# Kernel tuning notes

Measured on AMD Instinct MI355X. Metric: run time of the kernel, lower is better.

Reference implementation:

```python
import jax, jax.numpy as jnp
import numpy as np
import math

PS = 16            # patch size for SigmaPredictor
HID = 8            # hidden_dim
SCALE = HID ** -0.5
SIGMA_CAP = 6.0    # BoundedSoftplus threshold
EPS_S = 1e-6       # BoundedSoftplus eps


def setup_inputs() -> dict:
    key = jax.random.key(0)
    ks = jax.random.split(key, 10)
    B, C, H, W = 2, 1, 384, 384
    d_in = C * PS * PS  # 256
    r = lambda k_, sh: jax.random.normal(k_, sh, dtype=jnp.float32) * 0.1
    z = lambda sh: jnp.zeros(sh, dtype=jnp.float32)
    return {
        "x": jax.random.uniform(ks[0], (B, C, H, W), dtype=jnp.float32),
        "Wq": r(ks[1], (d_in, HID)), "bq": z((HID,)),
        "Wk": r(ks[2], (d_in, HID)), "bk": z((HID,)),
        "Wv": r(ks[3], (d_in, HID)), "bv": z((HID,)),
        "Wsq": r(ks[4], (HID, HID)), "bsq": z((HID,)),
        "Wsk": r(ks[5], (HID, HID)), "bsk": z((HID,)),
        "Wsv": r(ks[6], (HID, HID)), "bsv": z((HID,)),
        "ln_g": jnp.ones((HID,), jnp.float32), "ln_b": z((HID,)),
        "Wp": r(ks[7], (HID, 3)),
        # bias ~4 -> sigmas ~4 -> kernel size k=13 (production-scale support)
        "bp": jnp.full((3,), 4.0, dtype=jnp.float32),
    }


def _attn(q, k, v):
    a = jax.nn.softmax(jnp.einsum('bnd,bmd->bnm', q, k) * SCALE, axis=-1)
    return jnp.einsum('bnm,bmd->bnd', a, v)


def _predict_sigmas(x, Wq, bq, Wk, bk, Wv, bv, Wsq, bsq, Wsk, bsk, Wsv, bsv, ln_g, ln_b, Wp, bp):
    b, c, h, w = x.shape
    Hp, Wn = h // PS, w // PS
    # unfold into non-overlapping patches: [B, Hp*Wn, C*PS*PS]
    pat = x.reshape(b, c, Hp, PS, Wn, PS).transpose(0, 2, 4, 1, 3, 5).reshape(b, Hp * Wn, c * PS * PS)
    feats = _attn(pat @ Wq + bq, pat @ Wk + bk, pat @ Wv + bv)
    o = _attn(feats @ Wsq + bsq, feats @ Wsk + bsk, feats @ Wsv + bsv)
    mu = o.mean(-1, keepdims=True)
    var = ((o - mu) ** 2).mean(-1, keepdims=True)
    o = (o - mu) / jnp.sqrt(var + 1e-5) * ln_g + ln_b
    s = jnp.minimum(jax.nn.softplus(o @ Wp + bp), SIGMA_CAP) + EPS_S  # BoundedSoftplus
    s = s.reshape(b, Hp, Wn, 3)
    # nearest-neighbor upsample to full resolution: [B, H, W, 3]
    return jnp.repeat(jnp.repeat(s, PS, axis=1), PS, axis=2)


def _bilateral(x, s, k):
    b, c, h, w = x.shape
    sx, sy, sr = s[..., 0], s[..., 1], s[..., 2]
    half = k // 2
    xp = jnp.pad(x, ((0, 0), (0, 0), (half, half), (half, half)))
    # [B, C, H, W, k*k], dy-major to match torch unfold/meshgrid ordering
    patches = jnp.stack([xp[:, :, dy:dy + h, dx:dx + w]
                         for dy in range(k) for dx in range(k)], axis=-1)
    coords = jnp.arange(-half, half + 1, dtype=jnp.float32)
    yy, xx = jnp.meshgrid(coords, coords, indexing='ij')
    xx2 = (xx ** 2).reshape(-1)
    yy2 = (yy ** 2).reshape(-1)
    # spatial kernel [B, H, W, k*k]
    sp = jnp.exp(-xx2 / (2 * sx[..., None] ** 2) - yy2 / (2 * sy[..., None] ** 2))
    # range kernel (C == 1 branch) [B, C, H, W, k*k]
    rg = jnp.exp(-(x[..., None] - patches) ** 2 / (2 * sr[:, None, :, :, None] ** 2))
    comb = sp[:, None] * rg
    norm = comb / (comb.sum(-1, keepdims=True) + 1e-8)
    return (patches * norm).sum(-1)


def reference(x, Wq, bq, Wk, bk, Wv, bv, Wsq, bsq, Wsk, bsk, Wsv, bsv, ln_g, ln_b, Wp, bp):
    s = _predict_sigmas(x, Wq, bq, Wk, bk, Wv, bv, Wsq, bsq, Wsk, bsk, Wsv, bsv, ln_g, ln_b, Wp, bp)
    # data-dependent kernel size, computed eagerly (matches torch .item())
    m = float(jnp.maximum(s[..., 0].max(), s[..., 1].max()))
    k = int(2 * math.ceil(m + 1))
    if k % 2 == 0:
        k += 1
    return _bilateral(x, s, k)
```

## Files before the change

### kernel.cpp

```cpp
#include <hip/hip_runtime.h>

#define N_TOK 576
#define HP    24
#define PS    16
#define IMG   384
#define ATTN_SCALE 0.35355339059327373f

__global__ __launch_bounds__(256) void k_qkv1(
    const float* __restrict__ x,
    const float* __restrict__ Wq, const float* __restrict__ bq,
    const float* __restrict__ Wk, const float* __restrict__ bk,
    const float* __restrict__ Wv, const float* __restrict__ bv,
    float* __restrict__ q1, float* __restrict__ k1, float* __restrict__ v1)
{
    const int blk = blockIdx.x;
    const int b  = blk / N_TOK;
    const int n  = blk % N_TOK;
    const int py = n / HP, px = n % HP;
    const int t  = threadIdx.x;
    const int iy = t >> 4, ix = t & 15;

    const float pv = x[b*IMG*IMG + (py*PS + iy)*IMG + (px*PS + ix)];

    float acc[24];
#pragma unroll
    for (int h = 0; h < 8; ++h) {
        acc[h]      = pv * Wq[t*8 + h];
        acc[8 + h]  = pv * Wk[t*8 + h];
        acc[16 + h] = pv * Wv[t*8 + h];
    }
#pragma unroll
    for (int off = 32; off > 0; off >>= 1) {
#pragma unroll
        for (int j = 0; j < 24; ++j)
            acc[j] += __shfl_down(acc[j], off);
    }
    __shared__ float red[4][24];
    const int lane = t & 63, w = t >> 6;
    if (lane == 0) {
#pragma unroll
        for (int j = 0; j < 24; ++j) red[w][j] = acc[j];
    }
    __syncthreads();
    if (t < 24) {
        float s = red[0][t] + red[1][t] + red[2][t] + red[3][t];
        const int h = t & 7, mat = t >> 3;
        const float* bias = (mat == 0) ? bq : (mat == 1) ? bk : bv;
        float* dst = (mat == 0) ? q1 : (mat == 1) ? k1 : v1;
        dst[(b*N_TOK + n)*8 + h] = s + bias[h];
    }
}

__global__ __launch_bounds__(256) void k_attn1(
    const float* __restrict__ q1, const float* __restrict__ k1, const float* __restrict__ v1,
    const float* __restrict__ Wsq, const float* __restrict__ bsq,
    const float* __restrict__ Wsk, const float* __restrict__ bsk,
    const float* __restrict__ Wsv, const float* __restrict__ bsv,
    float* __restrict__ q2, float* __restrict__ k2, float* __restrict__ v2)
{
    const int lane = threadIdx.x & 63;
    const int wv   = threadIdx.x >> 6;
    const int tok  = blockIdx.x*4 + wv;
    const int b    = tok / N_TOK;

    float qv[8];
#pragma unroll
    for (int h = 0; h < 8; ++h) qv[h] = q1[tok*8 + h];

    const float* kb = k1 + b*N_TOK*8;
    const float* vb = v1 + b*N_TOK*8;

    float sc[9], mx = -1e30f;
#pragma unroll
    for (int ch = 0; ch < 9; ++ch) {
        const float* kp = kb + (ch*64 + lane)*8;
        float d = 0.f;
#pragma unroll
        for (int h = 0; h < 8; ++h) d += qv[h]*kp[h];
        d *= ATTN_SCALE;
        sc[ch] = d;
        mx = fmaxf(mx, d);
    }
#pragma unroll
    for (int off = 32; off > 0; off >>= 1) mx = fmaxf(mx, __shfl_xor(mx, off));

    float ssum = 0.f, o[8];
#pragma unroll
    for (int h = 0; h < 8; ++h) o[h] = 0.f;
#pragma unroll
    for (int ch = 0; ch < 9; ++ch) {
        const float p = __expf(sc[ch] - mx);
        ssum += p;
        const float* vp = vb + (ch*64 + lane)*8;
#pragma unroll
        for (int h = 0; h < 8; ++h) o[h] += p*vp[h];
    }
#pragma unroll
    for (int off = 32; off > 0; off >>= 1) {
        ssum += __shfl_xor(ssum, off);
#pragma unroll
        for (int h = 0; h < 8; ++h) o[h] += __shfl_xor(o[h], off);
    }
    const float inv = 1.f/ssum;
    float f[8];
#pragma unroll
    for (int h = 0; h < 8; ++h) f[h] = o[h]*inv;

    if (lane < 24) {
        const int mat = lane >> 3, h = lane & 7;
        const float* Wm = (mat==0)?Wsq:(mat==1)?Wsk:Wsv;
        const float* bm = (mat==0)?bsq:(mat==1)?bsk:bsv;
        float s = bm[h];
#pragma unroll
        for (int j = 0; j < 8; ++j) s += f[j]*Wm[j*8 + h];
        float* dst = (mat==0)?q2:(mat==1)?k2:v2;
        dst[tok*8 + h] = s;
    }
}

__global__ __launch_bounds__(256) void k_attn2(
    const float* __restrict__ q2, const float* __restrict__ k2, const float* __restrict__ v2,
    const float* __restrict__ ln_g, const float* __restrict__ ln_b,
    const float* __restrict__ Wp,   const float* __restrict__ bp,
    float* __restrict__ sig, int* __restrict__ smax)
{
    const int lane = threadIdx.x & 63;
    const int wv   = threadIdx.x >> 6;
    const int tok  = blockIdx.x*4 + wv;
    const int b    = tok / N_TOK;

    float qv[8];
#pragma unroll
    for (int h = 0; h < 8; ++h) qv[h] = q2[tok*8 + h];

    const float* kb = k2 + b*N_TOK*8;
    const float* vb = v2 + b*N_TOK*8;

    float sc[9], mx = -1e30f;
#pragma unroll
    for (int ch = 0; ch < 9; ++ch) {
        const float* kp = kb + (ch*64 + lane)*8;
        float d = 0.f;
#pragma unroll
        for (int h = 0; h < 8; ++h) d += qv[h]*kp[h];
        d *= ATTN_SCALE;
        sc[ch] = d;
        mx = fmaxf(mx, d);
    }
#pragma unroll
    for (int off = 32; off > 0; off >>= 1) mx = fmaxf(mx, __shfl_xor(mx, off));

    float ssum = 0.f, o[8];
#pragma unroll
    for (int h = 0; h < 8; ++h) o[h] = 0.f;
#pragma unroll
    for (int ch = 0; ch < 9; ++ch) {
        const float p = __expf(sc[ch] - mx);
        ssum += p;
        const float* vp = vb + (ch*64 + lane)*8;
#pragma unroll
        for (int h = 0; h < 8; ++h) o[h] += p*vp[h];
    }
#pragma unroll
    for (int off = 32; off > 0; off >>= 1) {
        ssum += __shfl_xor(ssum, off);
#pragma unroll
        for (int h = 0; h < 8; ++h) o[h] += __shfl_xor(o[h], off);
    }

    if (lane == 0) {
        const float inv = 1.f/ssum;
        float f[8];
        float mu = 0.f;
#pragma unroll
        for (int h = 0; h < 8; ++h) { f[h] = o[h]*inv; mu += f[h]; }
        mu *= 0.125f;
        float var = 0.f;
#pragma unroll
        for (int h = 0; h < 8; ++h) { const float d = f[h]-mu; var += d*d; }
        var *= 0.125f;
        const float rinv = rsqrtf(var + 1e-5f);
        float on[8];
#pragma unroll
        for (int h = 0; h < 8; ++h)
            on[h] = (f[h]-mu)*rinv*ln_g[h] + ln_b[h];
        float sv[3];
#pragma unroll
        for (int c = 0; c < 3; ++c) {
            float z = bp[c];
#pragma unroll
            for (int j = 0; j < 8; ++j) z += on[j]*Wp[j*3 + c];
            const float sp = (z > 20.f) ? z : log1pf(__expf(z));
            sv[c] = fminf(sp, 6.0f) + 1e-6f;
            sig[tok*3 + c] = sv[c];
        }
        atomicMax(smax, __float_as_int(fmaxf(sv[0], sv[1])));
    }
}

__global__ void k_half(const int* __restrict__ smaxi, int* __restrict__ halfp)
{
    const float m = __int_as_float(*smaxi);
    int h = (int)ceilf(m + 1.0f);
    if (h < 1) h = 1;
    if (h > 8) h = 8;
    halfp[0] = h;
}

__global__ __launch_bounds__(256) void k_bilat(
    const float* __restrict__ x, const float* __restrict__ sig,
    const int* __restrict__ halfp, float* __restrict__ out)
{
    __shared__ float tile[32*40];
    const int blk = blockIdx.x;
    const int b  = blk / N_TOK;
    const int n  = blk % N_TOK;
    const int py = n / HP, px = n % HP;
    const int tx = threadIdx.x & 15, ty = threadIdx.x >> 4;

    const int half = halfp[0];
    const float sx = sig[blk*3 + 0];
    const float sy = sig[blk*3 + 1];
    const float sr = sig[blk*3 + 2];

    const int tilew = PS + 2*half;
    const float* xb = x + b*IMG*IMG;
    for (int yy = ty; yy < tilew; yy += 16) {
        const int gy = py*PS + yy - half;
        for (int xx = tx; xx < tilew; xx += 16) {
            const int gx = px*PS + xx - half;
            float v = 0.f;
            if ((unsigned)gy < IMG && (unsigned)gx < IMG)
                v = xb[gy*IMG + gx];
            tile[yy*40 + xx] = v;
        }
    }
    __syncthreads();

    const float c  = tile[(ty+half)*40 + (tx+half)];
    const float ax = -0.5f/(sx*sx);
    const float ay = -0.5f/(sy*sy);
    const float ar = -0.5f/(sr*sr);

    float num = 0.f, den = 0.f;
    const int k = 2*half + 1;
    for (int dy = 0; dy < k; ++dy) {
        const float fy = (float)(dy - half);
        const float ey = ay*fy*fy;
        const float* row = &tile[(ty+dy)*40 + tx];
        for (int dx = 0; dx < k; ++dx) {
            const float fx = (float)(dx - half);
            const float p  = row[dx];
            const float d  = c - p;
            const float w  = __expf(ey + ax*fx*fx + ar*d*d);
            den += w;
            num += w*p;
        }
    }
    out[b*IMG*IMG + (py*PS + ty)*IMG + (px*PS + tx)] = num/(den + 1e-8f);
}

extern "C" void kernel_launch(void* const* d_in, const int* in_sizes, int n_in,
                              void* d_out, int out_size, void* d_ws, size_t ws_size,
                              hipStream_t stream)
{
    const float* x    = (const float*)d_in[0];
    const float* Wq   = (const float*)d_in[1];
    const float* bq   = (const float*)d_in[2];
    const float* Wk   = (const float*)d_in[3];
    const float* bk   = (const float*)d_in[4];
    const float* Wv   = (const float*)d_in[5];
    const float* bv   = (const float*)d_in[6];
    const float* Wsq  = (const float*)d_in[7];
    const float* bsq  = (const float*)d_in[8];
    const float* Wsk  = (const float*)d_in[9];
    const float* bsk  = (const float*)d_in[10];
    const float* Wsv  = (const float*)d_in[11];
    const float* bsv  = (const float*)d_in[12];
    const float* ln_g = (const float*)d_in[13];
    const float* ln_b = (const float*)d_in[14];
    const float* Wp   = (const float*)d_in[15];
    const float* bp   = (const float*)d_in[16];

    float* W  = (float*)d_ws;
    float* q1 = W;
    float* k1 = W +  9216;
    float* v1 = W + 18432;
    float* q2 = W + 27648;
    float* k2 = W + 36864;
    float* v2 = W + 46080;
    float* sg = W + 55296;
    int* smax = (int*)(W + 58752);
    int* halfp = smax + 1;

    hipMemsetAsync(smax, 0, 2*sizeof(int), stream);

    k_qkv1<<<2*N_TOK, 256, 0, stream>>>(x, Wq, bq, Wk, bk, Wv, bv, q1, k1, v1);
    k_attn1<<<2*N_TOK/4, 256, 0, stream>>>(q1, k1, v1, Wsq, bsq, Wsk, bsk, Wsv, bsv,
                                           q2, k2, v2);
    k_attn2<<<2*N_TOK/4, 256, 0, stream>>>(q2, k2, v2, ln_g, ln_b, Wp, bp, sg, smax);
    k_half<<<1, 1, 0, stream>>>(smax, halfp);
    k_bilat<<<2*N_TOK, 256, 0, stream>>>(x, sg, halfp, (float*)d_out);
}
```

Before: 143.0 us.

## Fuse sigma predictor and bilateral filter into one cooperative kernel with grid syncs

Replaces the five-launch pipeline (memset, qkv, two attention stages, half computation, bilateral) with a single cooperative kernel of 576 blocks. Each block handles one patch position for both batches and uses grid.sync between stages. The bilateral stage also precomputes the spatial Gaussian into shared memory and uses exp2f for the range term. This removes launch overhead and intermediate round trips, at the cost of grid-wide barriers and fewer blocks with more serial work each. A fallback keeps the multi-kernel path, which now resets smax inside k_qkv1 and computes half inside k_bilat, if the cooperative launch fails.

```diff
diff --git a/kernel.cpp b/kernel.cpp
--- a/kernel.cpp
+++ b/kernel.cpp
@@ -1,4 +1,7 @@
 #include <hip/hip_runtime.h>
+#include <hip/hip_cooperative_groups.h>
+
+namespace cg = cooperative_groups;
 
 #define N_TOK 576
 #define HP    24
@@ -6,12 +9,242 @@
 #define IMG   384
 #define ATTN_SCALE 0.35355339059327373f
 
+struct Params {
+    const float *x;
+    const float *Wq, *bq, *Wk, *bk, *Wv, *bv;
+    const float *Wsq, *bsq, *Wsk, *bsk, *Wsv, *bsv;
+    const float *ln_g, *ln_b, *Wp, *bp;
+    float *q1, *k1, *v1, *q2, *k2, *v2;
+    int  *smax;
+    float *out;
+};
+
+__device__ __forceinline__ void block_attn(
+    const float* __restrict__ qrow, const float* __restrict__ kb,
+    const float* __restrict__ vb, float* lds, float f[8])
+{
+    const int t = threadIdx.x, lane = t & 63, wv = t >> 6;
+    float qv[8];
+#pragma unroll
+    for (int h = 0; h < 8; ++h) qv[h] = qrow[h];
+
+    float sc[3], mx = -1e30f;
+#pragma unroll
+    for (int r = 0; r < 3; ++r) {
+        const int idx = t + r*256;
+        if (idx < N_TOK) {
+            const float* kp = kb + idx*8;
+            float d = 0.f;
+#pragma unroll
+            for (int h = 0; h < 8; ++h) d += qv[h]*kp[h];
+            sc[r] = d * ATTN_SCALE;
+            mx = fmaxf(mx, sc[r]);
+        }
+    }
+#pragma unroll
+    for (int off = 32; off; off >>= 1) mx = fmaxf(mx, __shfl_xor(mx, off));
+    if (lane == 0) lds[wv] = mx;
+    __syncthreads();
+    mx = fmaxf(fmaxf(lds[0], lds[1]), fmaxf(lds[2], lds[3]));
+
+    float o[9];
+#pragma unroll
+    for (int j = 0; j < 9; ++j) o[j] = 0.f;
+#pragma unroll
+    for (int r = 0; r < 3; ++r) {
+        const int idx = t + r*256;
+        if (idx < N_TOK) {
+            const float pw = __expf(sc[r] - mx);
+            o[8] += pw;
+            const float* vp = vb + idx*8;
+#pragma unroll
+            for (int h = 0; h < 8; ++h) o[h] += pw*vp[h];
+        }
+    }
+#pragma unroll
+    for (int off = 32; off; off >>= 1)
+#pragma unroll
+        for (int j = 0; j < 9; ++j) o[j] += __shfl_xor(o[j], off);
+    if (lane == 0)
+#pragma unroll
+        for (int j = 0; j < 9; ++j) lds[4 + wv*9 + j] = o[j];
+    __syncthreads();
+    float tot[9];
+#pragma unroll
+    for (int j = 0; j < 9; ++j)
+        tot[j] = lds[4+j] + lds[13+j] + lds[22+j] + lds[31+j];
+    const float inv = 1.f / tot[8];
+#pragma unroll
+    for (int h = 0; h < 8; ++h) f[h] = tot[h]*inv;
+    __syncthreads();
+}
+
+__global__ __launch_bounds__(256, 4) void k_fused(Params p)
+{
+    __shared__ float lds[1572];
+    __shared__ float s_sig[2][3];
+    __shared__ int   s_half;
+
+    const int t = threadIdx.x;
+    const int lane = t & 63, wv = t >> 6;
+    const int n = blockIdx.x;
+    const int py = n / HP, px = n % HP;
+
+    cg::grid_group grid = cg::this_grid();
+
+    if (n == 0 && t == 0) *p.smax = 0;
+    {
+        const int iy = t >> 4, ix = t & 15;
+#pragma unroll
+        for (int bi = 0; bi < 2; ++bi) {
+            const float pv = p.x[bi*IMG*IMG + (py*PS + iy)*IMG + (px*PS + ix)];
+            float acc[24];
+#pragma unroll
+            for (int h = 0; h < 8; ++h) {
+                acc[h]      = pv * p.Wq[t*8 + h];
+                acc[8 + h]  = pv * p.Wk[t*8 + h];
+                acc[16 + h] = pv * p.Wv[t*8 + h];
+            }
+#pragma unroll
+            for (int off = 32; off; off >>= 1)
+#pragma unroll
+                for (int j = 0; j < 24; ++j) acc[j] += __shfl_down(acc[j], off);
+            if (lane == 0)
+#pragma unroll
+                for (int j = 0; j < 24; ++j) lds[wv*24 + j] = acc[j];
+            __syncthreads();
+            if (t < 24) {
+                const float s = lds[t] + lds[24+t] + lds[48+t] + lds[72+t];
+                const int h = t & 7, mat = t >> 3;
+                const float* bias = (mat==0) ? p.bq : (mat==1) ? p.bk : p.bv;
+                float* dst = (mat==0) ? p.q1 : (mat==1) ? p.k1 : p.v1;
+                dst[(bi*N_TOK + n)*8 + h] = s + bias[h];
+            }
+            __syncthreads();
+        }
+    }
+    grid.sync();
+
+#pragma unroll
+    for (int bi = 0; bi < 2; ++bi) {
+        const int tok = bi*N_TOK + n;
+        float f[8];
+        block_attn(p.q1 + tok*8, p.k1 + bi*N_TOK*8, p.v1 + bi*N_TOK*8, lds, f);
+        if (t < 24) {
+            const int mat = t >> 3, h = t & 7;
+            const float* Wm = (mat==0)?p.Wsq:(mat==1)?p.Wsk:p.Wsv;
+            const float* bm = (mat==0)?p.bsq:(mat==1)?p.bsk:p.bsv;
+            float s = bm[h];
+#pragma unroll
+            for (int j = 0; j < 8; ++j) s += f[j]*Wm[j*8 + h];
+            float* dst = (mat==0)?p.q2:(mat==1)?p.k2:p.v2;
+            dst[tok*8 + h] = s;
+        }
+    }
+    grid.sync();
+
+#pragma unroll
+    for (int bi = 0; bi < 2; ++bi) {
+        const int tok = bi*N_TOK + n;
+        float f[8];
+        block_attn(p.q2 + tok*8, p.k2 + bi*N_TOK*8, p.v2 + bi*N_TOK*8, lds, f);
+        if (t == 0) {
+            float mu = 0.f;
+#pragma unroll
+            for (int h = 0; h < 8; ++h) mu += f[h];
+            mu *= 0.125f;
+            float var = 0.f;
+#pragma unroll
+            for (int h = 0; h < 8; ++h) { const float d = f[h]-mu; var += d*d; }
+            var *= 0.125f;
+            const float rinv = rsqrtf(var + 1e-5f);
+            float on[8];
+#pragma unroll
+            for (int h = 0; h < 8; ++h)
+                on[h] = (f[h]-mu)*rinv*p.ln_g[h] + p.ln_b[h];
+            float sv[3];
+#pragma unroll
+            for (int c = 0; c < 3; ++c) {
+                float z = p.bp[c];
+#pragma unroll
+                for (int j = 0; j < 8; ++j) z += on[j]*p.Wp[j*3 + c];
+                const float sp = (z > 20.f) ? z : log1pf(__expf(z));
+                sv[c] = fminf(sp, 6.0f) + 1e-6f;
+                s_sig[bi][c] = sv[c];
+            }
+            atomicMax(p.smax, __float_as_int(fmaxf(sv[0], sv[1])));
+        }
+    }
+    grid.sync();
+
+    {
+        if (t == 0) {
+            const int mi = atomicMax(p.smax, 0);
+            const float m = __int_as_float(mi);
+            int h = (int)ceilf(m + 1.0f);
+            if (h < 1) h = 1;
+            if (h > 8) h = 8;
+            s_half = h;
+        }
+        __syncthreads();
+        const int half = s_half;
+        const int k = 2*half + 1;
+        const int tilew = PS + 2*half;
+        const int tx = t & 15, ty = t >> 4;
+        float* tile = lds;
+        float* spt  = lds + 1280;
+
+        for (int bi = 0; bi < 2; ++bi) {
+            const float sx = s_sig[bi][0], sy = s_sig[bi][1], sr = s_sig[bi][2];
+            const float* xb = p.x + bi*IMG*IMG;
+
+            for (int yy = ty; yy < tilew; yy += 16) {
+                const int gy = py*PS + yy - half;
+                for (int xx = tx; xx < tilew; xx += 16) {
+                    const int gx = px*PS + xx - half;
+                    float v = 0.f;
+                    if ((unsigned)gy < IMG && (unsigned)gx < IMG)
+                        v = xb[gy*IMG + gx];
+                    tile[yy*40 + xx] = v;
+                }
+            }
+            const float axc = -0.5f/(sx*sx);
+            const float ayc = -0.5f/(sy*sy);
+            for (int i = t; i < k*k; i += 256) {
+                const int dy = i / k, dx = i - dy*k;
+                const float fy = (float)(dy - half), fx = (float)(dx - half);
+                spt[i] = __expf(ayc*fy*fy + axc*fx*fx);
+            }
+            __syncthreads();
+
+            const float c   = tile[(ty+half)*40 + (tx+half)];
+            const float ar2 = -0.72134752044448170f/(sr*sr);
+            float num = 0.f, den = 0.f;
+            for (int dy = 0; dy < k; ++dy) {
+                const float* row = &tile[(ty+dy)*40 + tx];
+                const float* spr = &spt[dy*k];
+                for (int dx = 0; dx < k; ++dx) {
+                    const float pix = row[dx];
+                    const float d   = c - pix;
+                    const float w   = spr[dx] * exp2f(ar2*d*d);
+                    den += w;
+                    num += w*pix;
+                }
+            }
+            p.out[bi*IMG*IMG + (py*PS + ty)*IMG + (px*PS + tx)] =
+                num/(den + 1e-8f);
+            __syncthreads();
+        }
+    }
+}
+
 __global__ __launch_bounds__(256) void k_qkv1(
     const float* __restrict__ x,
     const float* __restrict__ Wq, const float* __restrict__ bq,
     const float* __restrict__ Wk, const float* __restrict__ bk,
     const float* __restrict__ Wv, const float* __restrict__ bv,
-    float* __restrict__ q1, float* __restrict__ k1, float* __restrict__ v1)
+    float* __restrict__ q1, float* __restrict__ k1, float* __restrict__ v1,
+    int* __restrict__ smax)
 {
     const int blk = blockIdx.x;
     const int b  = blk / N_TOK;
@@ -20,6 +253,8 @@
     const int t  = threadIdx.x;
     const int iy = t >> 4, ix = t & 15;
 
+    if (blk == 0 && t == 0) *smax = 0;
+
     const float pv = x[b*IMG*IMG + (py*PS + iy)*IMG + (px*PS + ix)];
 
     float acc[24];
@@ -30,17 +265,14 @@
         acc[16 + h] = pv * Wv[t*8 + h];
     }
 #pragma unroll
-    for (int off = 32; off > 0; off >>= 1) {
-#pragma unroll
-        for (int j = 0; j < 24; ++j)
-            acc[j] += __shfl_down(acc[j], off);
-    }
+    for (int off = 32; off; off >>= 1)
+#pragma unroll
+        for (int j = 0; j < 24; ++j) acc[j] += __shfl_down(acc[j], off);
     __shared__ float red[4][24];
     const int lane = t & 63, w = t >> 6;
-    if (lane == 0) {
+    if (lane == 0)
 #pragma unroll
         for (int j = 0; j < 24; ++j) red[w][j] = acc[j];
-    }
     __syncthreads();
     if (t < 24) {
         float s = red[0][t] + red[1][t] + red[2][t] + red[3][t];
@@ -66,7 +298,6 @@
     float qv[8];
 #pragma unroll
     for (int h = 0; h < 8; ++h) qv[h] = q1[tok*8 + h];
-
     const float* kb = k1 + b*N_TOK*8;
     const float* vb = v1 + b*N_TOK*8;
 
@@ -82,21 +313,21 @@
         mx = fmaxf(mx, d);
     }
 #pragma unroll
-    for (int off = 32; off > 0; off >>= 1) mx = fmaxf(mx, __shfl_xor(mx, off));
+    for (int off = 32; off; off >>= 1) mx = fmaxf(mx, __shfl_xor(mx, off));
 
     float ssum = 0.f, o[8];
 #pragma unroll
     for (int h = 0; h < 8; ++h) o[h] = 0.f;
 #pragma unroll
     for (int ch = 0; ch < 9; ++ch) {
-        const float p = __expf(sc[ch] - mx);
-        ssum += p;
+        const float pw = __expf(sc[ch] - mx);
+        ssum += pw;
         const float* vp = vb + (ch*64 + lane)*8;
 #pragma unroll
-        for (int h = 0; h < 8; ++h) o[h] += p*vp[h];
-    }
-#pragma unroll
-    for (int off = 32; off > 0; off >>= 1) {
+        for (int h = 0; h < 8; ++h) o[h] += pw*vp[h];
+    }
+#pragma unroll
+    for (int off = 32; off; off >>= 1) {
         ssum += __shfl_xor(ssum, off);
 #pragma unroll
         for (int h = 0; h < 8; ++h) o[h] += __shfl_xor(o[h], off);
@@ -132,7 +363,6 @@
     float qv[8];
 #pragma unroll
     for (int h = 0; h < 8; ++h) qv[h] = q2[tok*8 + h];
-
     const float* kb = k2 + b*N_TOK*8;
     const float* vb = v2 + b*N_TOK*8;
 
@@ -148,21 +378,21 @@
         mx = fmaxf(mx, d);
     }
 #pragma unroll
-    for (int off = 32; off > 0; off >>= 1) mx = fmaxf(mx, __shfl_xor(mx, off));
+    for (int off = 32; off; off >>= 1) mx = fmaxf(mx, __shfl_xor(mx, off));
 
     float ssum = 0.f, o[8];
 #pragma unroll
     for (int h = 0; h < 8; ++h) o[h] = 0.f;
 #pragma unroll
     for (int ch = 0; ch < 9; ++ch) {
-        const float p = __expf(sc[ch] - mx);
-        ssum += p;
+        const float pw = __expf(sc[ch] - mx);
+        ssum += pw;
         const float* vp = vb + (ch*64 + lane)*8;
 #pragma unroll
-        for (int h = 0; h < 8; ++h) o[h] += p*vp[h];
-    }
-#pragma unroll
-    for (int off = 32; off > 0; off >>= 1) {
+        for (int h = 0; h < 8; ++h) o[h] += pw*vp[h];
+    }
+#pragma unroll
+    for (int off = 32; off; off >>= 1) {
         ssum += __shfl_xor(ssum, off);
 #pragma unroll
         for (int h = 0; h < 8; ++h) o[h] += __shfl_xor(o[h], off);
@@ -198,27 +428,27 @@
     }
 }
 
-__global__ void k_half(const int* __restrict__ smaxi, int* __restrict__ halfp)
-{
-    const float m = __int_as_float(*smaxi);
-    int h = (int)ceilf(m + 1.0f);
-    if (h < 1) h = 1;
-    if (h > 8) h = 8;
-    halfp[0] = h;
-}
-
 __global__ __launch_bounds__(256) void k_bilat(
     const float* __restrict__ x, const float* __restrict__ sig,
-    const int* __restrict__ halfp, float* __restrict__ out)
+    int* __restrict__ smax, float* __restrict__ out)
 {
     __shared__ float tile[32*40];
+    __shared__ int s_half;
     const int blk = blockIdx.x;
     const int b  = blk / N_TOK;
     const int n  = blk % N_TOK;
     const int py = n / HP, px = n % HP;
     const int tx = threadIdx.x & 15, ty = threadIdx.x >> 4;
 
-    const int half = halfp[0];
+    if (threadIdx.x == 0) {
+        const float m = __int_as_float(atomicMax(smax, 0));
+        int h = (int)ceilf(m + 1.0f);
+        if (h < 1) h = 1;
+        if (h > 8) h = 8;
+        s_half = h;
+    }
+    __syncthreads();
+    const int half = s_half;
     const float sx = sig[blk*3 + 0];
     const float sy = sig[blk*3 + 1];
     const float sr = sig[blk*3 + 2];
@@ -250,11 +480,11 @@
         const float* row = &tile[(ty+dy)*40 + tx];
         for (int dx = 0; dx < k; ++dx) {
             const float fx = (float)(dx - half);
-            const float p  = row[dx];
-            const float d  = c - p;
+            const float pix = row[dx];
+            const float d  = c - pix;
             const float w  = __expf(ey + ax*fx*fx + ar*d*d);
             den += w;
-            num += w*p;
+            num += w*pix;
         }
     }
     out[b*IMG*IMG + (py*PS + ty)*IMG + (px*PS + tx)] = num/(den + 1e-8f);
@@ -264,41 +494,49 @@
                               void* d_out, int out_size, void* d_ws, size_t ws_size,
                               hipStream_t stream)
 {
-    const float* x    = (const float*)d_in[0];
-    const float* Wq   = (const float*)d_in[1];
-    const float* bq   = (const float*)d_in[2];
-    const float* Wk   = (const float*)d_in[3];
-    const float* bk   = (const float*)d_in[4];
-    const float* Wv   = (const float*)d_in[5];
-    const float* bv   = (const float*)d_in[6];
-    const float* Wsq  = (const float*)d_in[7];
-    const float* bsq  = (const float*)d_in[8];
-    const float* Wsk  = (const float*)d_in[9];
-    const float* bsk  = (const float*)d_in[10];
-    const float* Wsv  = (const float*)d_in[11];
-    const float* bsv  = (const float*)d_in[12];
-    const float* ln_g = (const float*)d_in[13];
-    const float* ln_b = (const float*)d_in[14];
-    const float* Wp   = (const float*)d_in[15];
-    const float* bp   = (const float*)d_in[16];
-
-    float* W  = (float*)d_ws;
-    float* q1 = W;
-    float* k1 = W +  9216;
-    float* v1 = W + 18432;
-    float* q2 = W + 27648;
-    float* k2 = W + 36864;
-    float* v2 = W + 46080;
+    Params p;
+    p.x    = (const float*)d_in[0];
+    p.Wq   = (const float*)d_in[1];
+    p.bq   = (const float*)d_in[2];
+    p.Wk   = (const float*)d_in[3];
+    p.bk   = (const float*)d_in[4];
+    p.Wv   = (const float*)d_in[5];
+    p.bv   = (const float*)d_in[6];
+    p.Wsq  = (const float*)d_in[7];
+    p.bsq  = (const float*)d_in[8];
+    p.Wsk  = (const float*)d_in[9];
+    p.bsk  = (const float*)d_in[10];
+    p.Wsv  = (const float*)d_in[11];
+    p.bsv  = (const float*)d_in[12];
+    p.ln_g = (const float*)d_in[13];
+    p.ln_b = (const float*)d_in[14];
+    p.Wp   = (const float*)d_in[15];
+    p.bp   = (const float*)d_in[16];
+
+    float* W = (float*)d_ws;
+    p.q1 = W;
+    p.k1 = W +  9216;
+    p.v1 = W + 18432;
+    p.q2 = W + 27648;
+    p.k2 = W + 36864;
+    p.v2 = W + 46080;
     float* sg = W + 55296;
-    int* smax = (int*)(W + 58752);
-    int* halfp = smax + 1;
-
-    hipMemsetAsync(smax, 0, 2*sizeof(int), stream);
-
-    k_qkv1<<<2*N_TOK, 256, 0, stream>>>(x, Wq, bq, Wk, bk, Wv, bv, q1, k1, v1);
-    k_attn1<<<2*N_TOK/4, 256, 0, stream>>>(q1, k1, v1, Wsq, bsq, Wsk, bsk, Wsv, bsv,
-                                           q2, k2, v2);
-    k_attn2<<<2*N_TOK/4, 256, 0, stream>>>(q2, k2, v2, ln_g, ln_b, Wp, bp, sg, smax);
-    k_half<<<1, 1, 0, stream>>>(smax, halfp);
-    k_bilat<<<2*N_TOK, 256, 0, stream>>>(x, sg, halfp, (float*)d_out);
-}
+    p.smax = (int*)(W + 58752);
+    p.out  = (float*)d_out;
+
+    void* args[] = { &p };
+    hipError_t err = hipLaunchCooperativeKernel((void*)k_fused, dim3(N_TOK),
+                                                dim3(256), args, 0, stream);
+    if (err != hipSuccess) {
+        k_qkv1<<<2*N_TOK, 256, 0, stream>>>(p.x, p.Wq, p.bq, p.Wk, p.bk,
+                                            p.Wv, p.bv, p.q1, p.k1, p.v1,
+                                            p.smax);
+        k_attn1<<<2*N_TOK/4, 256, 0, stream>>>(p.q1, p.k1, p.v1,
+                                               p.Wsq, p.bsq, p.Wsk, p.bsk,
+                                               p.Wsv, p.bsv, p.q2, p.k2, p.v2);
+        k_attn2<<<2*N_TOK/4, 256, 0, stream>>>(p.q2, p.k2, p.v2,
+                                               p.ln_g, p.ln_b, p.Wp, p.bp,
+                                               sg, p.smax);
+        k_bilat<<<2*N_TOK, 256, 0, stream>>>(p.x, sg, p.smax, p.out);
+    }
+}
```

After: 324.1 us. +126.6%, slower.

## Drop memset and half-size kernel, remap QKV to one wave per patch, precompute spatial weights

Applied to the files above, without the earlier changes.

Removes the memset and the single-thread k_half launch: smax is reset inside k_qkv1 and the kernel half-width is computed per block in k_bilat. k_qkv1 now assigns one wavefront per patch with float4 loads and an xor-shuffle reduction, dropping the shared-memory step and the block barrier. The attention kernels use float4 loads for q, k and v. k_bilat precomputes the spatial Gaussian into shared memory and uses exp2f for the range term, removing one exp argument term per tap. The smax reset inside k_qkv1 relies on k_qkv1 finishing before k_attn2 runs its atomics, which stream ordering provides.

```diff
diff --git a/kernel.cpp b/kernel.cpp
--- a/kernel.cpp
+++ b/kernel.cpp
@@ -11,43 +11,47 @@
     const float* __restrict__ Wq, const float* __restrict__ bq,
     const float* __restrict__ Wk, const float* __restrict__ bk,
     const float* __restrict__ Wv, const float* __restrict__ bv,
-    float* __restrict__ q1, float* __restrict__ k1, float* __restrict__ v1)
-{
-    const int blk = blockIdx.x;
-    const int b  = blk / N_TOK;
-    const int n  = blk % N_TOK;
+    float* __restrict__ q1, float* __restrict__ k1, float* __restrict__ v1,
+    int* __restrict__ smax)
+{
+    const int lane = threadIdx.x & 63, wv = threadIdx.x >> 6;
+    const int idx = blockIdx.x*4 + wv;
+    const int b = idx / N_TOK, n = idx % N_TOK;
     const int py = n / HP, px = n % HP;
-    const int t  = threadIdx.x;
-    const int iy = t >> 4, ix = t & 15;
-
-    const float pv = x[b*IMG*IMG + (py*PS + iy)*IMG + (px*PS + ix)];
+
+    if (idx == 0 && lane == 0) atomicExch(smax, 0);
+
+    const int iy = lane >> 2, ix0 = (lane & 3) * 4;
+    const float4 pv = *(const float4*)
+        &x[b*IMG*IMG + (py*PS + iy)*IMG + px*PS + ix0];
 
     float acc[24];
 #pragma unroll
-    for (int h = 0; h < 8; ++h) {
-        acc[h]      = pv * Wq[t*8 + h];
-        acc[8 + h]  = pv * Wk[t*8 + h];
-        acc[16 + h] = pv * Wv[t*8 + h];
-    }
-#pragma unroll
-    for (int off = 32; off > 0; off >>= 1) {
-#pragma unroll
-        for (int j = 0; j < 24; ++j)
-            acc[j] += __shfl_down(acc[j], off);
-    }
-    __shared__ float red[4][24];
-    const int lane = t & 63, w = t >> 6;
+    for (int j = 0; j < 24; ++j) acc[j] = 0.f;
+
+#pragma unroll
+    for (int j = 0; j < 4; ++j) {
+        const int t = 4*lane + j;
+        const float p = ((const float*)&pv)[j];
+#pragma unroll
+        for (int h = 0; h < 8; ++h) {
+            acc[h]      += p * Wq[t*8 + h];
+            acc[8 + h]  += p * Wk[t*8 + h];
+            acc[16 + h] += p * Wv[t*8 + h];
+        }
+    }
+#pragma unroll
+    for (int off = 32; off; off >>= 1)
+#pragma unroll
+        for (int j = 0; j < 24; ++j) acc[j] += __shfl_xor(acc[j], off);
+
     if (lane == 0) {
 #pragma unroll
-        for (int j = 0; j < 24; ++j) red[w][j] = acc[j];
-    }
-    __syncthreads();
-    if (t < 24) {
-        float s = red[0][t] + red[1][t] + red[2][t] + red[3][t];
-        const int h = t & 7, mat = t >> 3;
-        const float* bias = (mat == 0) ? bq : (mat == 1) ? bk : bv;
-        float* dst = (mat == 0) ? q1 : (mat == 1) ? k1 : v1;
-        dst[(b*N_TOK + n)*8 + h] = s + bias[h];
+        for (int h = 0; h < 8; ++h) {
+            q1[idx*8 + h] = acc[h]      + bq[h];
+            k1[idx*8 + h] = acc[8 + h]  + bk[h];
+            v1[idx*8 + h] = acc[16 + h] + bv[h];
+        }
     }
 }
 
@@ -63,26 +67,25 @@
     const int tok  = blockIdx.x*4 + wv;
     const int b    = tok / N_TOK;
 
-    float qv[8];
-#pragma unroll
-    for (int h = 0; h < 8; ++h) qv[h] = q1[tok*8 + h];
-
-    const float* kb = k1 + b*N_TOK*8;
-    const float* vb = v1 + b*N_TOK*8;
+    const float4 qa = *(const float4*)&q1[tok*8];
+    const float4 qb = *(const float4*)&q1[tok*8 + 4];
+
+    const float* kbp = k1 + b*N_TOK*8;
+    const float* vbp = v1 + b*N_TOK*8;
 
     float sc[9], mx = -1e30f;
 #pragma unroll
     for (int ch = 0; ch < 9; ++ch) {
-        const float* kp = kb + (ch*64 + lane)*8;
-        float d = 0.f;
-#pragma unroll
-        for (int h = 0; h < 8; ++h) d += qv[h]*kp[h];
+        const float4* kp = (const float4*)(kbp + (ch*64 + lane)*8);
+        const float4 k0 = kp[0], k1v = kp[1];
+        float d = qa.x*k0.x + qa.y*k0.y + qa.z*k0.z + qa.w*k0.w
+                + qb.x*k1v.x + qb.y*k1v.y + qb.z*k1v.z + qb.w*k1v.w;
         d *= ATTN_SCALE;
         sc[ch] = d;
         mx = fmaxf(mx, d);
     }
 #pragma unroll
-    for (int off = 32; off > 0; off >>= 1) mx = fmaxf(mx, __shfl_xor(mx, off));
+    for (int off = 32; off; off >>= 1) mx = fmaxf(mx, __shfl_xor(mx, off));
 
     float ssum = 0.f, o[8];
 #pragma unroll
@@ -91,12 +94,13 @@
     for (int ch = 0; ch < 9; ++ch) {
         const float p = __expf(sc[ch] - mx);
         ssum += p;
-        const float* vp = vb + (ch*64 + lane)*8;
-#pragma unroll
-        for (int h = 0; h < 8; ++h) o[h] += p*vp[h];
-    }
-#pragma unroll
-    for (int off = 32; off > 0; off >>= 1) {
+        const float4* vp = (const float4*)(vbp + (ch*64 + lane)*8);
+        const float4 v0 = vp[0], v1v = vp[1];
+        o[0] += p*v0.x; o[1] += p*v0.y; o[2] += p*v0.z; o[3] += p*v0.w;
+        o[4] += p*v1v.x; o[5] += p*v1v.y; o[6] += p*v1v.z; o[7] += p*v1v.w;
+    }
+#pragma unroll
+    for (int off = 32; off; off >>= 1) {
         ssum += __shfl_xor(ssum, off);
 #pragma unroll
         for (int h = 0; h < 8; ++h) o[h] += __shfl_xor(o[h], off);
@@ -129,26 +133,25 @@
     const int tok  = blockIdx.x*4 + wv;
     const int b    = tok / N_TOK;
 
-    float qv[8];
-#pragma unroll
-    for (int h = 0; h < 8; ++h) qv[h] = q2[tok*8 + h];
-
-    const float* kb = k2 + b*N_TOK*8;
-    const float* vb = v2 + b*N_TOK*8;
+    const float4 qa = *(const float4*)&q2[tok*8];
+    const float4 qb = *(const float4*)&q2[tok*8 + 4];
+
+    const float* kbp = k2 + b*N_TOK*8;
+    const float* vbp = v2 + b*N_TOK*8;
 
     float sc[9], mx = -1e30f;
 #pragma unroll
     for (int ch = 0; ch < 9; ++ch) {
-        const float* kp = kb + (ch*64 + lane)*8;
-        float d = 0.f;
-#pragma unroll
-        for (int h = 0; h < 8; ++h) d += qv[h]*kp[h];
+        const float4* kp = (const float4*)(kbp + (ch*64 + lane)*8);
+        const float4 k0 = kp[0], k1v = kp[1];
+        float d = qa.x*k0.x + qa.y*k0.y + qa.z*k0.z + qa.w*k0.w
+                + qb.x*k1v.x + qb.y*k1v.y + qb.z*k1v.z + qb.w*k1v.w;
         d *= ATTN_SCALE;
         sc[ch] = d;
         mx = fmaxf(mx, d);
     }
 #pragma unroll
-    for (int off = 32; off > 0; off >>= 1) mx = fmaxf(mx, __shfl_xor(mx, off));
+    for (int off = 32; off; off >>= 1) mx = fmaxf(mx, __shfl_xor(mx, off));
 
     float ssum = 0.f, o[8];
 #pragma unroll
@@ -157,12 +160,13 @@
     for (int ch = 0; ch < 9; ++ch) {
         const float p = __expf(sc[ch] - mx);
         ssum += p;
-        const float* vp = vb + (ch*64 + lane)*8;
-#pragma unroll
-        for (int h = 0; h < 8; ++h) o[h] += p*vp[h];
-    }
-#pragma unroll
-    for (int off = 32; off > 0; off >>= 1) {
+        const float4* vp = (const float4*)(vbp + (ch*64 + lane)*8);
+        const float4 v0 = vp[0], v1v = vp[1];
+        o[0] += p*v0.x; o[1] += p*v0.y; o[2] += p*v0.z; o[3] += p*v0.w;
+        o[4] += p*v1v.x; o[5] += p*v1v.y; o[6] += p*v1v.z; o[7] += p*v1v.w;
+    }
+#pragma unroll
+    for (int off = 32; off; off >>= 1) {
         ssum += __shfl_xor(ssum, off);
 #pragma unroll
         for (int h = 0; h < 8; ++h) o[h] += __shfl_xor(o[h], off);
@@ -198,32 +202,36 @@
     }
 }
 
-__global__ void k_half(const int* __restrict__ smaxi, int* __restrict__ halfp)
-{
-    const float m = __int_as_float(*smaxi);
-    int h = (int)ceilf(m + 1.0f);
-    if (h < 1) h = 1;
-    if (h > 8) h = 8;
-    halfp[0] = h;
-}
-
 __global__ __launch_bounds__(256) void k_bilat(
     const float* __restrict__ x, const float* __restrict__ sig,
-    const int* __restrict__ halfp, float* __restrict__ out)
+    int* __restrict__ smax, float* __restrict__ out)
 {
     __shared__ float tile[32*40];
+    __shared__ float spt[17*17];
+    __shared__ int   s_half;
+
     const int blk = blockIdx.x;
     const int b  = blk / N_TOK;
     const int n  = blk % N_TOK;
     const int py = n / HP, px = n % HP;
     const int tx = threadIdx.x & 15, ty = threadIdx.x >> 4;
 
-    const int half = halfp[0];
+    if (threadIdx.x == 0) {
+        const float m = __int_as_float(atomicMax(smax, 0));
+        int h = (int)ceilf(m + 1.0f);
+        if (h < 1) h = 1;
+        if (h > 8) h = 8;
+        s_half = h;
+    }
+    __syncthreads();
+    const int half = s_half;
+    const int k = 2*half + 1;
+    const int tilew = PS + 2*half;
+
     const float sx = sig[blk*3 + 0];
     const float sy = sig[blk*3 + 1];
     const float sr = sig[blk*3 + 2];
 
-    const int tilew = PS + 2*half;
     const float* xb = x + b*IMG*IMG;
     for (int yy = ty; yy < tilew; yy += 16) {
         const int gy = py*PS + yy - half;
@@ -235,26 +243,30 @@
             tile[yy*40 + xx] = v;
         }
     }
+    {
+        const float axc = -0.5f/(sx*sx);
+        const float ayc = -0.5f/(sy*sy);
+        for (int i = threadIdx.x; i < k*k; i += 256) {
+            const int dy = i / k, dx = i - dy*k;
+            const float fy = (float)(dy - half), fx = (float)(dx - half);
+            spt[i] = __expf(ayc*fy*fy + axc*fx*fx);
+        }
+    }
     __syncthreads();
 
-    const float c  = tile[(ty+half)*40 + (tx+half)];
-    const float ax = -0.5f/(sx*sx);
-    const float ay = -0.5f/(sy*sy);
-    const float ar = -0.5f/(sr*sr);
+    const float c   = tile[(ty+half)*40 + (tx+half)];
+    const float ar2 = -0.72134752044448170f/(sr*sr);
 
     float num = 0.f, den = 0.f;
-    const int k = 2*half + 1;
     for (int dy = 0; dy < k; ++dy) {
-        const float fy = (float)(dy - half);
-        const float ey = ay*fy*fy;
         const float* row = &tile[(ty+dy)*40 + tx];
+        const float* spr = &spt[dy*k];
         for (int dx = 0; dx < k; ++dx) {
-            const float fx = (float)(dx - half);
-            const float p  = row[dx];
-            const float d  = c - p;
-            const float w  = __expf(ey + ax*fx*fx + ar*d*d);
+            const float pix = row[dx];
+            const float d   = c - pix;
+            const float w   = spr[dx] * exp2f(ar2*d*d);
             den += w;
-            num += w*p;
+            num += w*pix;
         }
     }
     out[b*IMG*IMG + (py*PS + ty)*IMG + (px*PS + tx)] = num/(den + 1e-8f);
@@ -291,14 +303,12 @@
     float* v2 = W + 46080;
     float* sg = W + 55296;
     int* smax = (int*)(W + 58752);
-    int* halfp = smax + 1;
-
-    hipMemsetAsync(smax, 0, 2*sizeof(int), stream);
-
-    k_qkv1<<<2*N_TOK, 256, 0, stream>>>(x, Wq, bq, Wk, bk, Wv, bv, q1, k1, v1);
-    k_attn1<<<2*N_TOK/4, 256, 0, stream>>>(q1, k1, v1, Wsq, bsq, Wsk, bsk, Wsv, bsv,
-                                           q2, k2, v2);
-    k_attn2<<<2*N_TOK/4, 256, 0, stream>>>(q2, k2, v2, ln_g, ln_b, Wp, bp, sg, smax);
-    k_half<<<1, 1, 0, stream>>>(smax, halfp);
-    k_bilat<<<2*N_TOK, 256, 0, stream>>>(x, sg, halfp, (float*)d_out);
-}
+
+    k_qkv1<<<2*N_TOK/4, 256, 0, stream>>>(x, Wq, bq, Wk, bk, Wv, bv,
+                                          q1, k1, v1, smax);
+    k_attn1<<<2*N_TOK/4, 256, 0, stream>>>(q1, k1, v1, Wsq, bsq, Wsk, bsk,
+                                           Wsv, bsv, q2, k2, v2);
+    k_attn2<<<2*N_TOK/4, 256, 0, stream>>>(q2, k2, v2, ln_g, ln_b, Wp, bp,
+                                           sg, smax);
+    k_bilat<<<2*N_TOK, 256, 0, stream>>>(x, sg, smax, (float*)d_out);
+}
```

After: 149.6 us. 1.05x slower.
